# Kernel tuning notes

Hardware: AMD Instinct MI355X
Metric: run time of the kernel (lower is better)

Reference implementation:

```python
import jax, jax.numpy as jnp
import numpy as np

N_COEFS = 128  # module init arg n_coefs


def _autocorr(x, n_coefs):
    # x: [B, L] -> normalized autocovariance coefficients [B, n_coefs+1]
    L = x.shape[1]
    com = L - n_coefs  # comparison window length
    # lagged windows: [n_coefs+1, com] index matrix
    idx = jnp.arange(n_coefs + 1)[:, None] + jnp.arange(com)[None, :]
    x0 = x[:, :com]
    x0c = x0 - jnp.mean(x0, axis=1, keepdims=True)          # [B, com]
    Y = x[:, idx]                                            # [B, n_coefs+1, com]
    Yc = Y - jnp.mean(Y, axis=2, keepdims=True)
    ac = jnp.mean(x0c[:, None, :] * Yc, axis=2)              # [B, n_coefs+1]
    # torch divides by c0 via .item() -> denominator is a constant
    c0 = jax.lax.stop_gradient(ac[:, :1])
    return ac / c0


def setup_inputs() -> dict:
    key = jax.random.key(0)
    k1, k2 = jax.random.split(key)
    B, C, L = 32, 1, 8192
    fake = jax.random.normal(k1, (B, C, L), dtype=jnp.float32)
    real = jax.random.normal(k2, (B, C, L), dtype=jnp.float32)
    return {"fake": fake, "real": real}


def reference(fake, real):
    B = fake.shape[0]
    L = fake.shape[2]
    f = fake.reshape(B, L)  # single channel
    r = real.reshape(B, L)
    fake_ac = _autocorr(f, N_COEFS)  # [B, n_coefs+1]
    real_ac = _autocorr(r, N_COEFS)
    return jnp.mean(jnp.abs(fake_ac - real_ac))  # L1Loss (mean)
```

## Files before the change

### kernel.cpp

```cpp
#include <hip/hip_runtime.h>

#define NC    129
#define LLEN  8192
#define COM   (LLEN - 128)
#define KTILE 16
#define NKT   9
#define BB    32

__global__ __launch_bounds__(256) void ac_sums_kernel(const float* __restrict__ fake,
                                                      const float* __restrict__ real,
                                                      float* __restrict__ S) {
    __shared__ float sx[8256];
    __shared__ float sred[64];

    const int tid   = threadIdx.x;
    const int ktile = blockIdx.x;
    const int b     = blockIdx.y;
    const int sig   = blockIdx.z;
    const float* x  = (sig == 0 ? fake : real) + (size_t)b * LLEN;

    float psum = 0.f;
#pragma unroll
    for (int i = 0; i < 8; ++i) {
        int g = tid + 256 * i;
        float4 v = reinterpret_cast<const float4*>(x)[g];
        reinterpret_cast<float4*>(sx)[g] = v;
        if (g < COM / 4) psum += (v.x + v.y) + (v.z + v.w);
    }
    if (tid < 64) sx[8192 + tid] = 0.f;

    for (int off = 1; off < 64; off <<= 1) psum += __shfl_xor(psum, off);
    if ((tid & 63) == 0) sred[tid >> 6] = psum;
    __syncthreads();
    const float mu = (sred[0] + sred[1] + sred[2] + sred[3]) * (1.0f / COM);

    const int k0 = ktile * KTILE;
    float acc[KTILE];
#pragma unroll
    for (int k = 0; k < KTILE; ++k) acc[k] = 0.f;

    for (int i = 0; i < 8; ++i) {
        int g = tid + 256 * i;
        if (g < COM / 4) {
            float4 x0 = reinterpret_cast<const float4*>(sx)[g];
            const float c0 = x0.x - mu, c1 = x0.y - mu, c2 = x0.z - mu, c3 = x0.w - mu;
            float w[20];
            const int base = 4 * g + k0;
#pragma unroll
            for (int j = 0; j < 5; ++j) {
                float4 wv = *reinterpret_cast<const float4*>(&sx[base + 4 * j]);
                w[4 * j + 0] = wv.x; w[4 * j + 1] = wv.y;
                w[4 * j + 2] = wv.z; w[4 * j + 3] = wv.w;
            }
#pragma unroll
            for (int k = 0; k < KTILE; ++k) {
                acc[k] = fmaf(c0, w[k + 0], acc[k]);
                acc[k] = fmaf(c1, w[k + 1], acc[k]);
                acc[k] = fmaf(c2, w[k + 2], acc[k]);
                acc[k] = fmaf(c3, w[k + 3], acc[k]);
            }
        }
    }

#pragma unroll
    for (int k = 0; k < KTILE; ++k)
        for (int off = 1; off < 64; off <<= 1) acc[k] += __shfl_xor(acc[k], off);

    __syncthreads();
    const int wave = tid >> 6, lane = tid & 63;
    if (lane == 0) {
#pragma unroll
        for (int k = 0; k < KTILE; ++k) sred[wave * KTILE + k] = acc[k];
    }
    __syncthreads();
    if (tid < KTILE) {
        int gk = k0 + tid;
        if (gk < NC) {
            float s = sred[tid] + sred[KTILE + tid] + sred[2 * KTILE + tid] + sred[3 * KTILE + tid];
            S[((size_t)sig * BB + b) * NC + gk] = s;
        }
    }
}

__global__ __launch_bounds__(256) void loss_kernel(const float* __restrict__ S,
                                                   float* __restrict__ out) {
    __shared__ float sred[4];
    const float* Sf = S;
    const float* Sr = S + (size_t)BB * NC;
    const int tid = threadIdx.x;

    float a = 0.f;
    for (int idx = tid; idx < BB * NC; idx += 256) {
        int b = idx / NC;
        int k = idx - b * NC;
        float fr = Sf[b * NC + k] / Sf[b * NC];
        float rr = Sr[b * NC + k] / Sr[b * NC];
        a += fabsf(fr - rr);
    }
    for (int off = 1; off < 64; off <<= 1) a += __shfl_xor(a, off);
    if ((tid & 63) == 0) sred[tid >> 6] = a;
    __syncthreads();
    if (tid == 0) out[0] = (sred[0] + sred[1] + sred[2] + sred[3]) * (1.0f / (BB * NC));
}

extern "C" void kernel_launch(void* const* d_in, const int* in_sizes, int n_in,
                              void* d_out, int out_size, void* d_ws, size_t ws_size,
                              hipStream_t stream) {
    const float* fake = (const float*)d_in[0];
    const float* real = (const float*)d_in[1];
    float* S = (float*)d_ws;
    float* out = (float*)d_out;

    dim3 grid(NKT, BB, 2);
    ac_sums_kernel<<<grid, 256, 0, stream>>>(fake, real, S);
    loss_kernel<<<1, 256, 0, stream>>>(S, out);
}
```

Before: 77.57 us.

## Fuse loss reduction into autocorr kernel via last-block counter and retile lags

Merges the separate loss kernel into the main kernel: each block atomically increments a global counter and the last block computes the L1 loss, which removes one kernel launch. The lag tiling also changes to 8 tiles of 16 plus one overlapping extra lag (17 outputs per block) instead of 9 tiles of 16, so 512 blocks cover all 129 lags with no padding. It adds a memset before the launch, an atomic and fences, and more FMAs per element per block.

```diff
diff --git a/kernel.cpp b/kernel.cpp
--- a/kernel.cpp
+++ b/kernel.cpp
@@ -3,15 +3,19 @@
 #define NC    129
 #define LLEN  8192
 #define COM   (LLEN - 128)
-#define KTILE 16
-#define NKT   9
+#define KT    16
+#define KOUT  17
+#define NKT   8
 #define BB    32
+#define NBLOCKS (NKT * BB * 2)
 
-__global__ __launch_bounds__(256) void ac_sums_kernel(const float* __restrict__ fake,
-                                                      const float* __restrict__ real,
-                                                      float* __restrict__ S) {
-    __shared__ float sx[8256];
-    __shared__ float sred[64];
+__global__ __launch_bounds__(256)
+void ac_fused_kernel(const float* __restrict__ fake, const float* __restrict__ real,
+                     float* __restrict__ out, unsigned int* __restrict__ counter,
+                     float* __restrict__ S) {
+    __shared__ float sx[LLEN];
+    __shared__ float sred[4 * KOUT];
+    __shared__ int lastFlag;
 
     const int tid   = threadIdx.x;
     const int ktile = blockIdx.x;
@@ -27,18 +31,17 @@
         reinterpret_cast<float4*>(sx)[g] = v;
         if (g < COM / 4) psum += (v.x + v.y) + (v.z + v.w);
     }
-    if (tid < 64) sx[8192 + tid] = 0.f;
-
     for (int off = 1; off < 64; off <<= 1) psum += __shfl_xor(psum, off);
     if ((tid & 63) == 0) sred[tid >> 6] = psum;
     __syncthreads();
     const float mu = (sred[0] + sred[1] + sred[2] + sred[3]) * (1.0f / COM);
 
-    const int k0 = ktile * KTILE;
-    float acc[KTILE];
+    const int k0 = ktile * KT;
+    float acc[KOUT];
 #pragma unroll
-    for (int k = 0; k < KTILE; ++k) acc[k] = 0.f;
+    for (int k = 0; k < KOUT; ++k) acc[k] = 0.f;
 
+#pragma unroll
     for (int i = 0; i < 8; ++i) {
         int g = tid + 256 * i;
         if (g < COM / 4) {
@@ -53,51 +56,53 @@
                 w[4 * j + 2] = wv.z; w[4 * j + 3] = wv.w;
             }
 #pragma unroll
-            for (int k = 0; k < KTILE; ++k) {
-                acc[k] = fmaf(c0, w[k + 0], acc[k]);
-                acc[k] = fmaf(c1, w[k + 1], acc[k]);
-                acc[k] = fmaf(c2, w[k + 2], acc[k]);
-                acc[k] = fmaf(c3, w[k + 3], acc[k]);
+            for (int k = 0; k < KOUT; ++k) {
+                float t0 = fmaf(c0, w[k + 0], acc[k]);
+                t0       = fmaf(c1, w[k + 1], t0);
+                t0       = fmaf(c2, w[k + 2], t0);
+                acc[k]   = fmaf(c3, w[k + 3], t0);
             }
         }
     }
 
 #pragma unroll
-    for (int k = 0; k < KTILE; ++k)
+    for (int k = 0; k < KOUT; ++k)
         for (int off = 1; off < 64; off <<= 1) acc[k] += __shfl_xor(acc[k], off);
 
+    const int wave = tid >> 6, lane = tid & 63;
     __syncthreads();
-    const int wave = tid >> 6, lane = tid & 63;
     if (lane == 0) {
 #pragma unroll
-        for (int k = 0; k < KTILE; ++k) sred[wave * KTILE + k] = acc[k];
+        for (int k = 0; k < KOUT; ++k) sred[wave * KOUT + k] = acc[k];
     }
     __syncthreads();
-    if (tid < KTILE) {
-        int gk = k0 + tid;
-        if (gk < NC) {
-            float s = sred[tid] + sred[KTILE + tid] + sred[2 * KTILE + tid] + sred[3 * KTILE + tid];
-            S[((size_t)sig * BB + b) * NC + gk] = s;
-        }
+    if (tid < KOUT) {
+        float s = sred[tid] + sred[KOUT + tid] + sred[2 * KOUT + tid] + sred[3 * KOUT + tid];
+        S[((size_t)sig * BB + b) * NC + k0 + tid] = s;
     }
-}
 
-__global__ __launch_bounds__(256) void loss_kernel(const float* __restrict__ S,
-                                                   float* __restrict__ out) {
-    __shared__ float sred[4];
+    __threadfence();
+    __syncthreads();
+    if (tid == 0) {
+        unsigned int old = atomicAdd(counter, 1u);
+        lastFlag = (old == NBLOCKS - 1) ? 1 : 0;
+    }
+    __syncthreads();
+    if (!lastFlag) return;
+
+    __threadfence();
     const float* Sf = S;
     const float* Sr = S + (size_t)BB * NC;
-    const int tid = threadIdx.x;
-
     float a = 0.f;
     for (int idx = tid; idx < BB * NC; idx += 256) {
-        int b = idx / NC;
-        int k = idx - b * NC;
-        float fr = Sf[b * NC + k] / Sf[b * NC];
-        float rr = Sr[b * NC + k] / Sr[b * NC];
+        int bb = idx / NC;
+        int kk = idx - bb * NC;
+        float fr = Sf[bb * NC + kk] / Sf[bb * NC];
+        float rr = Sr[bb * NC + kk] / Sr[bb * NC];
         a += fabsf(fr - rr);
     }
     for (int off = 1; off < 64; off <<= 1) a += __shfl_xor(a, off);
+    __syncthreads();
     if ((tid & 63) == 0) sred[tid >> 6] = a;
     __syncthreads();
     if (tid == 0) out[0] = (sred[0] + sred[1] + sred[2] + sred[3]) * (1.0f / (BB * NC));
@@ -108,10 +113,11 @@
                               hipStream_t stream) {
     const float* fake = (const float*)d_in[0];
     const float* real = (const float*)d_in[1];
-    float* S = (float*)d_ws;
+    unsigned int* counter = (unsigned int*)d_ws;
+    float* S = (float*)((char*)d_ws + 256);
     float* out = (float*)d_out;
 
+    hipMemsetAsync(d_ws, 0, 4, stream);
     dim3 grid(NKT, BB, 2);
-    ac_sums_kernel<<<grid, 256, 0, stream>>>(fake, real, S);
-    loss_kernel<<<1, 256, 0, stream>>>(S, out);
+    ac_fused_kernel<<<grid, 256, 0, stream>>>(fake, real, out, counter, S);
 }
```

Result: slower. 105.6 us (+36.1%).
